# Optimization experiments

Hardware: AMD Instinct MI355X
Metric: run time of the kernel (lower is better)

## Reference

```python
import jax, jax.numpy as jnp
import numpy as np

E = 768
H = 12
D = E // H          # head_dim = 64
R = 4               # reduced_head_dim
SCALING = D ** -0.5  # scaling_factor = 1
B, T = 4, 1024


def setup_inputs() -> dict:
    key = jax.random.key(0)
    ks = jax.random.split(key, 12)
    query = jax.random.normal(ks[0], (B, T, E), dtype=jnp.float32)
    k_dynamic_T = jax.random.normal(ks[1], (B * H * T, R, T), dtype=jnp.float32)
    kpm = jax.random.bernoulli(ks[2], 0.2, (B, T))
    kpm = kpm.at[:, 0].set(False)  # keep at least one key unmasked per row
    attn_bias = jax.random.normal(ks[3], (B * H, T, T), dtype=jnp.float32)
    s_in = (2.0 / (E + 3 * E)) ** 0.5
    s_red = (2.0 / (D + R)) ** 0.5
    s_out = (2.0 / (E + E)) ** 0.5
    return {
        "query": query,
        "k_dynamic_T": k_dynamic_T,
        "key_padding_mask": kpm,
        "attn_bias": attn_bias,
        "in_w": jax.random.normal(ks[4], (3 * E, E), dtype=jnp.float32) * s_in,
        "in_b": jax.random.normal(ks[5], (3 * E,), dtype=jnp.float32) * 0.02,
        "red_w": jax.random.normal(ks[6], (R, D), dtype=jnp.float32) * s_red,
        "red_b": jax.random.normal(ks[7], (R,), dtype=jnp.float32) * 0.02,
        "out_w": jax.random.normal(ks[8], (E, E), dtype=jnp.float32) * s_out,
        "out_b": jax.random.normal(ks[9], (E,), dtype=jnp.float32) * 0.02,
    }


def reference(query, k_dynamic_T, key_padding_mask, attn_bias,
              in_w, in_b, red_w, red_b, out_w, out_b):
    bsz, tgt_len, _ = query.shape
    # QKV projection (torch Linear: x @ W.T + b)
    qkv = jnp.einsum("bte,fe->btf", query, in_w) + in_b
    q, k, v = jnp.split(qkv, 3, axis=-1)
    # [B, H, T, D]
    q = q.reshape(bsz, tgt_len, H, D).transpose(0, 2, 1, 3)
    k = k.reshape(bsz, tgt_len, H, D).transpose(0, 2, 1, 3)
    v = v.reshape(bsz, tgt_len, H, D).transpose(0, 2, 1, 3)
    # low-rank dynamic bias: q_reduced from UNSCALED q
    q_red = jnp.einsum("bhtd,rd->bhtr", q, red_w) + red_b          # [B,H,T,R]
    k_dyn = k_dynamic_T.reshape(bsz, H, tgt_len, R, tgt_len)       # [B,H,T,R,S]
    attn_dyn = jnp.einsum("bhtr,bhtrs->bhts", q_red, k_dyn)        # [B,H,T,S]
    # scaled dot-product scores + dynamic bias
    scores = jnp.einsum("bhtd,bhsd->bhts", q * SCALING, k) + attn_dyn
    # key padding mask -> -inf
    scores = jnp.where(key_padding_mask[:, None, None, :], -jnp.inf, scores)
    # attn_bias added inside softmax_dropout (bias arg); dropout inactive (eval)
    scores = scores + attn_bias.reshape(bsz, H, tgt_len, tgt_len)
    attn = jax.nn.softmax(scores, axis=-1)
    o = jnp.einsum("bhts,bhsd->bhtd", attn, v)                     # [B,H,T,D]
    o = o.transpose(0, 2, 1, 3).reshape(bsz, tgt_len, E)
    return jnp.einsum("bte,fe->btf", o, out_w) + out_b
```

## Files before the change

kernel.cpp:

```cpp
#include <hip/hip_runtime.h>
#include <math.h>

typedef __attribute__((ext_vector_type(8))) short s16x8;
typedef __attribute__((ext_vector_type(4))) float f32x4;

#define MFMA(a,b,c) __builtin_amdgcn_mfma_f32_16x16x32_bf16((a),(b),(c),0,0,0)

__device__ __forceinline__ unsigned short f2bf(float f){
    unsigned u = __builtin_bit_cast(unsigned, f);
    u += 0x7FFFu + ((u >> 16) & 1u);
    return (unsigned short)(u >> 16);
}
__device__ __forceinline__ float bf2f(unsigned short u){
    return __builtin_bit_cast(float, ((unsigned)u) << 16);
}
__device__ __forceinline__ float4 fma4(float s, float4 a, float4 c){
    c.x = fmaf(s, a.x, c.x); c.y = fmaf(s, a.y, c.y);
    c.z = fmaf(s, a.z, c.z); c.w = fmaf(s, a.w, c.w);
    return c;
}
__device__ __forceinline__ unsigned pk_bf16(float lo, float hi){
    return (unsigned)f2bf(lo) | ((unsigned)f2bf(hi) << 16);
}
__device__ __forceinline__ void gld_lds16(const void* g, void* l){
    __builtin_amdgcn_global_load_lds(
        (const __attribute__((address_space(1))) void*)g,
        (__attribute__((address_space(3))) void*)l, 16, 0, 0);
}

__global__ __launch_bounds__(256) void cvt3(
    const float* __restrict__ s0, unsigned short* __restrict__ d0, int n0,
    const float* __restrict__ s1, unsigned short* __restrict__ d1, int n1,
    const float* __restrict__ s2, unsigned short* __restrict__ d2, int n2)
{
    const int i = blockIdx.x*256 + threadIdx.x;
    const float* s; unsigned short* d; int j;
    if (i < n0){ s = s0; d = d0; j = i; }
    else if (i < n0 + n1){ s = s1; d = d1; j = i - n0; }
    else if (i < n0 + n1 + n2){ s = s2; d = d2; j = i - n0 - n1; }
    else return;
    float4 a = *(const float4*)(s + (size_t)j*8);
    float4 b = *(const float4*)(s + (size_t)j*8 + 4);
    alignas(16) unsigned short t[8] = {
        f2bf(a.x), f2bf(a.y), f2bf(a.z), f2bf(a.w),
        f2bf(b.x), f2bf(b.y), f2bf(b.z), f2bf(b.w) };
    *(s16x8*)(d + (size_t)j*8) = *(const s16x8*)t;
}

__global__ __launch_bounds__(256) void gemm_qkv_bf16(
    const unsigned short* __restrict__ X,
    const unsigned short* __restrict__ W,
    const float* __restrict__ bvec,
    unsigned short* __restrict__ qs,
    unsigned short* __restrict__ kb,
    unsigned short* __restrict__ vtb)
{
    __shared__ __align__(16) unsigned short Al[128*64];
    __shared__ __align__(16) unsigned short Bl[128*64];
    const int tid = threadIdx.x;
    const int m0 = blockIdx.y*128, n0 = blockIdx.x*128;
    const int w = tid>>6, lane = tid&63, g = lane>>4, cc = lane&15;
    const int arow_base = (w>>1)*64, brow_base = (w&1)*64;
    const int srowb = w*32 + (lane>>3);
    const int gl = lane&7;

    f32x4 acc[4][4];
#pragma unroll
    for (int i=0;i<4;i++)
#pragma unroll
        for (int j=0;j<4;j++) acc[i][j] = (f32x4){0.f,0.f,0.f,0.f};

    for (int kt = 0; kt < 768; kt += 64) {
        __syncthreads();
#pragma unroll
        for (int i=0;i<4;i++){
            const int ra = srowb + i*8;
            gld_lds16(X + (size_t)(m0+ra)*768 + kt + ((gl ^ (ra&7))<<3),
                      &Al[(w*32 + i*8)*64]);
            gld_lds16(W + (size_t)(n0+ra)*768 + kt + ((gl ^ (ra&7))<<3),
                      &Bl[(w*32 + i*8)*64]);
        }
        __syncthreads();
#pragma unroll
        for (int ks=0;ks<2;ks++){
            s16x8 af[4], bfr[4];
#pragma unroll
            for (int i=0;i<4;i++){
                const int ra = arow_base + i*16 + cc;
                const int rb = brow_base + i*16 + cc;
                af[i]  = *(const s16x8*)&Al[ra*64 + (((ks*4+g) ^ (ra&7))<<3)];
                bfr[i] = *(const s16x8*)&Bl[rb*64 + (((ks*4+g) ^ (rb&7))<<3)];
            }
#pragma unroll
            for (int i=0;i<4;i++)
#pragma unroll
                for (int j=0;j<4;j++)
                    acc[i][j] = MFMA(af[i], bfr[j], acc[i][j]);
        }
    }

    const int region = blockIdx.x / 6;
#pragma unroll
    for (int j=0;j<4;j++){
        const int n = n0 + brow_base + j*16 + cc;
        const float bb = bvec[n];
        const int nn = n - region*768;
        const int h = nn >> 6, d = nn & 63;
        if (region == 0){
#pragma unroll
            for (int i=0;i<4;i++){
                const int m = m0 + arow_base + i*16 + g*4;
                const int bq = m >> 10, t = m & 1023;
                unsigned short* dst = qs + ((size_t)(bq*12+h)*1024 + t)*64 + d;
#pragma unroll
                for (int r=0;r<4;r++)
                    dst[(size_t)r*64] = f2bf((acc[i][j][r] + bb)*0.125f);
            }
        } else if (region == 1){
#pragma unroll
            for (int i=0;i<4;i++){
                const int m = m0 + arow_base + i*16 + g*4;
                const int bq = m >> 10, t = m & 1023;
                unsigned short* dst = kb + ((size_t)(bq*12+h)*1024 + t)*64 + d;
#pragma unroll
                for (int r=0;r<4;r++)
                    dst[(size_t)r*64] = f2bf(acc[i][j][r] + bb);
            }
        } else {
#pragma unroll
            for (int i=0;i<4;i++){
                const int m = m0 + arow_base + i*16 + g*4;
                const int bq = m >> 10, t = m & 1023;
                ushort4 pk;
                pk.x = f2bf(acc[i][j][0] + bb);
                pk.y = f2bf(acc[i][j][1] + bb);
                pk.z = f2bf(acc[i][j][2] + bb);
                pk.w = f2bf(acc[i][j][3] + bb);
                *(ushort4*)&vtb[((size_t)(bq*12+h)*64 + d)*1024 + t] = pk;
            }
        }
    }
}

__global__ __launch_bounds__(256) void gemm_obf_bf16(
    const unsigned short* __restrict__ X,
    const unsigned short* __restrict__ W,
    const float* __restrict__ bvec, float* __restrict__ out)
{
    __shared__ __align__(16) unsigned short Al[128*64];
    __shared__ __align__(16) unsigned short Bl[128*64];
    const int tid = threadIdx.x;
    const int m0 = blockIdx.y*128, n0 = blockIdx.x*128;
    const int w = tid>>6, lane = tid&63, g = lane>>4, cc = lane&15;
    const int arow_base = (w>>1)*64, brow_base = (w&1)*64;
    const int srowb = w*32 + (lane>>3);
    const int gl = lane&7;

    f32x4 acc[4][4];
#pragma unroll
    for (int i=0;i<4;i++)
#pragma unroll
        for (int j=0;j<4;j++) acc[i][j] = (f32x4){0.f,0.f,0.f,0.f};

    for (int kt = 0; kt < 768; kt += 64) {
        __syncthreads();
#pragma unroll
        for (int i=0;i<4;i++){
            const int ra = srowb + i*8;
            gld_lds16(X + (size_t)(m0+ra)*768 + kt + ((gl ^ (ra&7))<<3),
                      &Al[(w*32 + i*8)*64]);
            gld_lds16(W + (size_t)(n0+ra)*768 + kt + ((gl ^ (ra&7))<<3),
                      &Bl[(w*32 + i*8)*64]);
        }
        __syncthreads();
#pragma unroll
        for (int ks=0;ks<2;ks++){
            s16x8 af[4], bfr[4];
#pragma unroll
            for (int i=0;i<4;i++){
                const int ra = arow_base + i*16 + cc;
                const int rb = brow_base + i*16 + cc;
                af[i]  = *(const s16x8*)&Al[ra*64 + (((ks*4+g) ^ (ra&7))<<3)];
                bfr[i] = *(const s16x8*)&Bl[rb*64 + (((ks*4+g) ^ (rb&7))<<3)];
            }
#pragma unroll
            for (int i=0;i<4;i++)
#pragma unroll
                for (int j=0;j<4;j++)
                    acc[i][j] = MFMA(af[i], bfr[j], acc[i][j]);
        }
    }
#pragma unroll
    for (int j=0;j<4;j++){
        const int n = n0 + brow_base + j*16 + cc;
        const float bb = bvec[n];
#pragma unroll
        for (int i=0;i<4;i++){
            const int mb = m0 + arow_base + i*16 + g*4;
#pragma unroll
            for (int r=0;r<4;r++)
                out[(size_t)(mb+r)*768 + n] = acc[i][j][r] + bb;
        }
    }
}

__global__ __launch_bounds__(64, 1) void attn_mfma(
    const unsigned short* __restrict__ qs,
    const unsigned short* __restrict__ kbf,
    const unsigned short* __restrict__ vtf,
    const float* __restrict__ kdyn,
    const int*   __restrict__ kpm,
    const float* __restrict__ bias,
    const float* __restrict__ red_w,
    const float* __restrict__ red_b,
    unsigned short* __restrict__ o)
{
    __shared__ __align__(16) float kdL[2][2048];
    __shared__ __align__(16) float bL[2][512];

    const int lane = threadIdx.x & 63;
    const int bh = blockIdx.x, qt = blockIdx.y;
    const int b = bh / 12, h = bh % 12;
    const int t0 = qt*16;
    const int g = lane>>4, cc = lane&15;
    const int tq = t0 + cc;

    const unsigned short* qrow = qs + ((size_t)bh*1024 + tq)*64;
    s16x8 qf[2];
    qf[0] = *(const s16x8*)(qrow + g*8);
    qf[1] = *(const s16x8*)(qrow + 32 + g*8);

    float qred[4];
    {
        float pr[4] = {0.f,0.f,0.f,0.f};
#pragma unroll
        for (int ks=0; ks<2; ks++){
#pragma unroll
            for (int r=0;r<4;r++){
                float4 w0 = *(const float4*)(red_w + r*64 + 32*ks + 8*g);
                float4 w1 = *(const float4*)(red_w + r*64 + 32*ks + 8*g + 4);
                pr[r] += bf2f((unsigned short)qf[ks][0])*w0.x + bf2f((unsigned short)qf[ks][1])*w0.y
                       + bf2f((unsigned short)qf[ks][2])*w0.z + bf2f((unsigned short)qf[ks][3])*w0.w
                       + bf2f((unsigned short)qf[ks][4])*w1.x + bf2f((unsigned short)qf[ks][5])*w1.y
                       + bf2f((unsigned short)qf[ks][6])*w1.z + bf2f((unsigned short)qf[ks][7])*w1.w;
            }
        }
#pragma unroll
        for (int r=0;r<4;r++){
            pr[r] += __shfl_xor(pr[r], 16);
            pr[r] += __shfl_xor(pr[r], 32);
            qred[r] = pr[r]*8.f + red_b[r];
        }
    }

    f32x4 accO[4];
#pragma unroll
    for (int i=0;i<4;i++) accO[i] = (f32x4){0.f,0.f,0.f,0.f};
    float m_ = -1e30f, l_ = 0.f;

    const unsigned short* kcb = kbf + (size_t)bh*1024*64;
    const unsigned short* vcb = vtf + ((size_t)bh*64 + cc)*1024;
    const int* mp = kpm + b*1024 + 4*g;
    const size_t kd_row = (size_t)(bh*1024 + t0);

    const int r8_ = lane>>3, g8_ = lane&7;

    #define STAGE(buf_, c_) do {                                                  \
        const int s0_ = (c_)*32;                                                  \
        _Pragma("unroll")                                                         \
        for (int i_=0;i_<8;i_++){                         \
            const int rr_ = 8*i_ + r8_;                                           \
            const int t_ = rr_>>2, r_ = rr_&3;                                    \
            gld_lds16(kdyn + (kd_row + t_)*4096 + (size_t)r_*1024 + s0_           \
                          + ((g8_ ^ (t_&7))<<2),                                  \
                      &kdL[buf_][i_*256]);                                        \
        }                                                                         \
        _Pragma("unroll")                                                         \
        for (int i_=0;i_<2;i_++){                          \
            const int t_ = 8*i_ + r8_;                                            \
            gld_lds16(bias + (kd_row + t_)*1024 + s0_ + ((g8_ ^ (t_&7))<<2),      \
                      &bL[buf_][i_*256]);                                         \
        }                                                                         \
    } while(0)

    STAGE(0, 0);

    const float NINF = -__builtin_inff();
    const int srcA = ((g&1)<<5) + cc;
    const int srcB = srcA + 16;
    const bool hi_half = (g>>1) != 0;

#pragma unroll 1
    for (int c = 0; c < 32; ++c) {
        const int buf = c & 1;
        const int s0 = c*32;

        s16x8 kfr[2][2];
#pragma unroll
        for (int sq=0;sq<2;sq++){
            const unsigned short* kp = kcb + (size_t)(s0 + 16*sq + cc)*64 + g*8;
            kfr[sq][0] = *(const s16x8*)(kp);
            kfr[sq][1] = *(const s16x8*)(kp + 32);
        }
        s16x8 vfr[4];
#pragma unroll
        for (int dq=0;dq<4;dq++)
            vfr[dq] = *(const s16x8*)(vcb + (size_t)dq*16*1024 + s0 + 8*g);
        int4 mm0 = *(const int4*)(mp + s0);
        int4 mm1 = *(const int4*)(mp + s0 + 16);
        __builtin_amdgcn_sched_barrier(0);

        if (c < 31){
            STAGE(buf^1, c+1);
            asm volatile("s_waitcnt vmcnt(10)" ::: "memory");
        } else {
            asm volatile("s_waitcnt vmcnt(0)" ::: "memory");
        }
        __builtin_amdgcn_sched_barrier(0);

        float4 dyn[2];
#pragma unroll
        for (int sq=0;sq<2;sq++){
            const int slot = ((4*sq + g) ^ (cc&7)) << 2;
            float4 dv = *(const float4*)&bL[buf][cc*32 + slot];
            dv = fma4(qred[0], *(const float4*)&kdL[buf][(cc*4+0)*32 + slot], dv);
            dv = fma4(qred[1], *(const float4*)&kdL[buf][(cc*4+1)*32 + slot], dv);
            dv = fma4(qred[2], *(const float4*)&kdL[buf][(cc*4+2)*32 + slot], dv);
            dv = fma4(qred[3], *(const float4*)&kdL[buf][(cc*4+3)*32 + slot], dv);
            const int4 m4 = sq ? mm1 : mm0;
            dv.x = m4.x ? NINF : dv.x;
            dv.y = m4.y ? NINF : dv.y;
            dv.z = m4.z ? NINF : dv.z;
            dv.w = m4.w ? NINF : dv.w;
            dyn[sq] = dv;
        }

        f32x4 sc[2];
        __builtin_amdgcn_s_setprio(1);
#pragma unroll
        for (int sq=0;sq<2;sq++){
            f32x4 z = (f32x4){0.f,0.f,0.f,0.f};
            z = MFMA(kfr[sq][0], qf[0], z);
            z = MFMA(kfr[sq][1], qf[1], z);
            sc[sq] = z;
        }
        __builtin_amdgcn_s_setprio(0);

        float v[8];
#pragma unroll
        for (int sq=0;sq<2;sq++){
            v[sq*4+0] = sc[sq][0] + dyn[sq].x;
            v[sq*4+1] = sc[sq][1] + dyn[sq].y;
            v[sq*4+2] = sc[sq][2] + dyn[sq].z;
            v[sq*4+3] = sc[sq][3] + dyn[sq].w;
        }
        float mx = v[0];
#pragma unroll
        for (int i=1;i<8;i++) mx = fmaxf(mx, v[i]);
        mx = fmaxf(mx, __shfl_xor(mx, 16));
        mx = fmaxf(mx, __shfl_xor(mx, 32));
        const float mn = fmaxf(m_, mx);
        float ps = 0.f;
#pragma unroll
        for (int i=0;i<8;i++){ v[i] = __expf(v[i]-mn); ps += v[i]; }
        ps += __shfl_xor(ps, 16);
        ps += __shfl_xor(ps, 32);
        const float scl = __expf(m_-mn);
        m_ = mn; l_ = l_*scl + ps;

        unsigned U[4] = { pk_bf16(v[0],v[1]), pk_bf16(v[2],v[3]),
                          pk_bf16(v[4],v[5]), pk_bf16(v[6],v[7]) };
        unsigned a0 = (unsigned)__shfl((int)U[0], srcA);
        unsigned a1 = (unsigned)__shfl((int)U[1], srcA);
        unsigned a2 = (unsigned)__shfl((int)U[2], srcA);
        unsigned a3 = (unsigned)__shfl((int)U[3], srcA);
        unsigned b0 = (unsigned)__shfl((int)U[0], srcB);
        unsigned b1 = (unsigned)__shfl((int)U[1], srcB);
        unsigned b2 = (unsigned)__shfl((int)U[2], srcB);
        unsigned b3 = (unsigned)__shfl((int)U[3], srcB);
        alignas(16) unsigned wv4[4] = { hi_half ? a2 : a0, hi_half ? a3 : a1,
                                        hi_half ? b2 : b0, hi_half ? b3 : b1 };
        s16x8 pa = *(const s16x8*)wv4;

        float sr[4];
#pragma unroll
        for (int r=0;r<4;r++) sr[r] = __shfl(scl, 20*g + r);
#pragma unroll
        for (int dq=0;dq<4;dq++){
            f32x4 a = accO[dq];
            a[0]*=sr[0]; a[1]*=sr[1]; a[2]*=sr[2]; a[3]*=sr[3];
            accO[dq] = a;
        }

        __builtin_amdgcn_s_setprio(1);
#pragma unroll
        for (int dq=0;dq<4;dq++)
            accO[dq] = MFMA(pa, vfr[dq], accO[dq]);
        __builtin_amdgcn_s_setprio(0);
    }
    #undef STAGE

    float linv[4];
#pragma unroll
    for (int r=0;r<4;r++) linv[r] = 1.0f / __shfl(l_, 20*g + r);
#pragma unroll
    for (int dq=0;dq<4;dq++){
#pragma unroll
        for (int r=0;r<4;r++){
            const int t = t0 + 4*g + r;
            o[(size_t)(b*1024 + t)*768 + h*64 + 16*dq + cc] = f2bf(accO[dq][r] * linv[r]);
        }
    }
}

extern "C" void kernel_launch(void* const* d_in, const int* in_sizes, int n_in,
                              void* d_out, int out_size, void* d_ws, size_t ws_size,
                              hipStream_t stream) {
    const float* query = (const float*)d_in[0];
    const float* kdyn  = (const float*)d_in[1];
    const int*   kpm   = (const int*)d_in[2];
    const float* bias  = (const float*)d_in[3];
    const float* in_w  = (const float*)d_in[4];
    const float* in_b  = (const float*)d_in[5];
    const float* red_w = (const float*)d_in[6];
    const float* red_b = (const float*)d_in[7];
    const float* out_w = (const float*)d_in[8];
    const float* out_b = (const float*)d_in[9];
    float* out = (float*)d_out;

    const size_t SEG = (size_t)48*1024*64;
    unsigned short* qs  = (unsigned short*)d_ws;
    unsigned short* kb  = qs + SEG;
    unsigned short* vt  = kb + SEG;
    unsigned short* ob  = vt + SEG;
    unsigned short* qb  = ob + SEG;
    unsigned short* wqb = qb + SEG;
    unsigned short* wob = wqb + (size_t)2304*768;

    const int n0 = (4096*768)/8;
    const int n1 = (2304*768)/8;
    const int n2 = (768*768)/8;
    cvt3<<<dim3((n0+n1+n2+255)/256), 256, 0, stream>>>(
        query, qb, n0, in_w, wqb, n1, out_w, wob, n2);

    gemm_qkv_bf16<<<dim3(18,32), 256, 0, stream>>>(qb, wqb, in_b, qs, kb, vt);
    attn_mfma<<<dim3(48,64), 64, 0, stream>>>(qs, kb, vt, kdyn, kpm, bias, red_w, red_b, ob);
    gemm_obf_bf16<<<dim3(6,32), 256, 0, stream>>>(ob, wob, out_b, out);
}
```

Measured before the change: 284.5 us.

## Double-buffer LDS tiles in QKV and output projection GEMMs

Both projection GEMMs now keep two LDS buffers per operand. The next k-tile is loaded directly into LDS while MFMAs run on the current one, synchronized with explicit vmcnt waits and barriers. This is meant to hide global-load latency behind compute, which the single-buffered loop exposed every iteration. LDS use per block doubles to 64 KB, which may lower occupancy. The hand-placed waitcnt counts also assume exactly 8 outstanding loads per stage.

```diff
diff --git a/kernel.cpp b/kernel.cpp
--- a/kernel.cpp
+++ b/kernel.cpp
@@ -55,8 +55,8 @@
     unsigned short* __restrict__ kb,
     unsigned short* __restrict__ vtb)
 {
-    __shared__ __align__(16) unsigned short Al[128*64];
-    __shared__ __align__(16) unsigned short Bl[128*64];
+    __shared__ __align__(16) unsigned short Al[2][128*64];
+    __shared__ __align__(16) unsigned short Bl[2][128*64];
     const int tid = threadIdx.x;
     const int m0 = blockIdx.y*128, n0 = blockIdx.x*128;
     const int w = tid>>6, lane = tid&63, g = lane>>4, cc = lane&15;
@@ -70,17 +70,28 @@
 #pragma unroll
         for (int j=0;j<4;j++) acc[i][j] = (f32x4){0.f,0.f,0.f,0.f};
 
-    for (int kt = 0; kt < 768; kt += 64) {
-        __syncthreads();
-#pragma unroll
-        for (int i=0;i<4;i++){
-            const int ra = srowb + i*8;
-            gld_lds16(X + (size_t)(m0+ra)*768 + kt + ((gl ^ (ra&7))<<3),
-                      &Al[(w*32 + i*8)*64]);
-            gld_lds16(W + (size_t)(n0+ra)*768 + kt + ((gl ^ (ra&7))<<3),
-                      &Bl[(w*32 + i*8)*64]);
-        }
-        __syncthreads();
+    #define GSTAGE(buf_, kt_) do {                                          \
+        _Pragma("unroll")                                                   \
+        for (int i_=0;i_<4;i_++){                                           \
+            const int ra_ = srowb + i_*8;                                   \
+            gld_lds16(X + (size_t)(m0+ra_)*768 + (kt_) + ((gl ^ (ra_&7))<<3), \
+                      &Al[buf_][(w*32 + i_*8)*64]);                         \
+            gld_lds16(W + (size_t)(n0+ra_)*768 + (kt_) + ((gl ^ (ra_&7))<<3), \
+                      &Bl[buf_][(w*32 + i_*8)*64]);                         \
+        }                                                                   \
+    } while(0)
+
+    GSTAGE(0, 0);
+    for (int step = 0; step < 12; ++step){
+        const int buf = step & 1;
+        if (step < 11){
+            GSTAGE(buf^1, (step+1)*64);
+            asm volatile("s_waitcnt vmcnt(8)" ::: "memory");
+        } else {
+            asm volatile("s_waitcnt vmcnt(0)" ::: "memory");
+        }
+        __builtin_amdgcn_s_barrier();
+        __builtin_amdgcn_sched_barrier(0);
 #pragma unroll
         for (int ks=0;ks<2;ks++){
             s16x8 af[4], bfr[4];
@@ -88,8 +99,8 @@
             for (int i=0;i<4;i++){
                 const int ra = arow_base + i*16 + cc;
                 const int rb = brow_base + i*16 + cc;
-                af[i]  = *(const s16x8*)&Al[ra*64 + (((ks*4+g) ^ (ra&7))<<3)];
-                bfr[i] = *(const s16x8*)&Bl[rb*64 + (((ks*4+g) ^ (rb&7))<<3)];
+                af[i]  = *(const s16x8*)&Al[buf][ra*64 + (((ks*4+g) ^ (ra&7))<<3)];
+                bfr[i] = *(const s16x8*)&Bl[buf][rb*64 + (((ks*4+g) ^ (rb&7))<<3)];
             }
 #pragma unroll
             for (int i=0;i<4;i++)
@@ -97,7 +108,10 @@
                 for (int j=0;j<4;j++)
                     acc[i][j] = MFMA(af[i], bfr[j], acc[i][j]);
         }
-    }
+        asm volatile("s_waitcnt lgkmcnt(0)" ::: "memory");
+        __builtin_amdgcn_s_barrier();
+    }
+    #undef GSTAGE
 
     const int region = blockIdx.x / 6;
 #pragma unroll
@@ -147,8 +161,8 @@
     const unsigned short* __restrict__ W,
     const float* __restrict__ bvec, float* __restrict__ out)
 {
-    __shared__ __align__(16) unsigned short Al[128*64];
-    __shared__ __align__(16) unsigned short Bl[128*64];
+    __shared__ __align__(16) unsigned short Al[2][128*64];
+    __shared__ __align__(16) unsigned short Bl[2][128*64];
     const int tid = threadIdx.x;
     const int m0 = blockIdx.y*128, n0 = blockIdx.x*128;
     const int w = tid>>6, lane = tid&63, g = lane>>4, cc = lane&15;
@@ -162,17 +176,28 @@
 #pragma unroll
         for (int j=0;j<4;j++) acc[i][j] = (f32x4){0.f,0.f,0.f,0.f};
 
-    for (int kt = 0; kt < 768; kt += 64) {
-        __syncthreads();
-#pragma unroll
-        for (int i=0;i<4;i++){
-            const int ra = srowb + i*8;
-            gld_lds16(X + (size_t)(m0+ra)*768 + kt + ((gl ^ (ra&7))<<3),
-                      &Al[(w*32 + i*8)*64]);
-            gld_lds16(W + (size_t)(n0+ra)*768 + kt + ((gl ^ (ra&7))<<3),
-                      &Bl[(w*32 + i*8)*64]);
-        }
-        __syncthreads();
+    #define GSTAGE(buf_, kt_) do {                                          \
+        _Pragma("unroll")                                                   \
+        for (int i_=0;i_<4;i_++){                                           \
+            const int ra_ = srowb + i_*8;                                   \
+            gld_lds16(X + (size_t)(m0+ra_)*768 + (kt_) + ((gl ^ (ra_&7))<<3), \
+                      &Al[buf_][(w*32 + i_*8)*64]);                         \
+            gld_lds16(W + (size_t)(n0+ra_)*768 + (kt_) + ((gl ^ (ra_&7))<<3), \
+                      &Bl[buf_][(w*32 + i_*8)*64]);                         \
+        }                                                                   \
+    } while(0)
+
+    GSTAGE(0, 0);
+    for (int step = 0; step < 12; ++step){
+        const int buf = step & 1;
+        if (step < 11){
+            GSTAGE(buf^1, (step+1)*64);
+            asm volatile("s_waitcnt vmcnt(8)" ::: "memory");
+        } else {
+            asm volatile("s_waitcnt vmcnt(0)" ::: "memory");
+        }
+        __builtin_amdgcn_s_barrier();
+        __builtin_amdgcn_sched_barrier(0);
 #pragma unroll
         for (int ks=0;ks<2;ks++){
             s16x8 af[4], bfr[4];
@@ -180,8 +205,8 @@
             for (int i=0;i<4;i++){
                 const int ra = arow_base + i*16 + cc;
                 const int rb = brow_base + i*16 + cc;
-                af[i]  = *(const s16x8*)&Al[ra*64 + (((ks*4+g) ^ (ra&7))<<3)];
-                bfr[i] = *(const s16x8*)&Bl[rb*64 + (((ks*4+g) ^ (rb&7))<<3)];
+                af[i]  = *(const s16x8*)&Al[buf][ra*64 + (((ks*4+g) ^ (ra&7))<<3)];
+                bfr[i] = *(const s16x8*)&Bl[buf][rb*64 + (((ks*4+g) ^ (rb&7))<<3)];
             }
 #pragma unroll
             for (int i=0;i<4;i++)
@@ -189,7 +214,11 @@
                 for (int j=0;j<4;j++)
                     acc[i][j] = MFMA(af[i], bfr[j], acc[i][j]);
         }
-    }
+        asm volatile("s_waitcnt lgkmcnt(0)" ::: "memory");
+        __builtin_amdgcn_s_barrier();
+    }
+    #undef GSTAGE
+
 #pragma unroll
     for (int j=0;j<4;j++){
         const int n = n0 + brow_base + j*16 + cc;
```

New measurement: 303.4 us. +6.7%, slower.

## Double-buffer K/V/mask register loads one chunk ahead in attention loop

Applied to the files above, without the earlier changes.

The K and V fragment loads and the key-padding mask loads move out of the current iteration and are prefetched into double-buffered registers for the next chunk, alongside the existing LDS staging of the dynamic-bias and attention-bias tiles. The waitcnt threshold is raised to cover the extra in-flight loads, so global latency for K/V overlaps with compute. The loop is unrolled by 2 so the register buffers can be indexed statically, and launch bounds now ask for 2 blocks per CU. The extra register buffers raise VGPR pressure and could cause spills or limit occupancy.

```diff
diff --git a/kernel.cpp b/kernel.cpp
--- a/kernel.cpp
+++ b/kernel.cpp
@@ -204,7 +204,7 @@
     }
 }
 
-__global__ __launch_bounds__(64, 1) void attn_mfma(
+__global__ __launch_bounds__(64, 2) void attn_mfma(
     const unsigned short* __restrict__ qs,
     const unsigned short* __restrict__ kbf,
     const unsigned short* __restrict__ vtf,
@@ -283,6 +283,26 @@
         }                                                                         \
     } while(0)
 
+    #define REGLOAD(p_, c_) do {                                                  \
+        const int s0n_ = (c_)*32;                                                 \
+        _Pragma("unroll")                                                         \
+        for (int sq_=0;sq_<2;sq_++){                                              \
+            const unsigned short* kp_ = kcb + (size_t)(s0n_ + 16*sq_ + cc)*64 + g*8; \
+            kfr[p_][sq_][0] = *(const s16x8*)(kp_);                               \
+            kfr[p_][sq_][1] = *(const s16x8*)(kp_ + 32);                          \
+        }                                                                         \
+        _Pragma("unroll")                                                         \
+        for (int dq_=0;dq_<4;dq_++)                                               \
+            vfr[p_][dq_] = *(const s16x8*)(vcb + (size_t)dq_*16*1024 + s0n_ + 8*g); \
+        mm0r[p_] = *(const int4*)(mp + s0n_);                                     \
+        mm1r[p_] = *(const int4*)(mp + s0n_ + 16);                                \
+    } while(0)
+
+    s16x8 kfr[2][2][2];
+    s16x8 vfr[2][4];
+    int4 mm0r[2], mm1r[2];
+
+    REGLOAD(0, 0);
     STAGE(0, 0);
 
     const float NINF = -__builtin_inff();
@@ -290,29 +310,14 @@
     const int srcB = srcA + 16;
     const bool hi_half = (g>>1) != 0;
 
-#pragma unroll 1
+#pragma unroll 2
     for (int c = 0; c < 32; ++c) {
-        const int buf = c & 1;
-        const int s0 = c*32;
-
-        s16x8 kfr[2][2];
-#pragma unroll
-        for (int sq=0;sq<2;sq++){
-            const unsigned short* kp = kcb + (size_t)(s0 + 16*sq + cc)*64 + g*8;
-            kfr[sq][0] = *(const s16x8*)(kp);
-            kfr[sq][1] = *(const s16x8*)(kp + 32);
-        }
-        s16x8 vfr[4];
-#pragma unroll
-        for (int dq=0;dq<4;dq++)
-            vfr[dq] = *(const s16x8*)(vcb + (size_t)dq*16*1024 + s0 + 8*g);
-        int4 mm0 = *(const int4*)(mp + s0);
-        int4 mm1 = *(const int4*)(mp + s0 + 16);
-        __builtin_amdgcn_sched_barrier(0);
+        const int pb = c & 1;
 
         if (c < 31){
-            STAGE(buf^1, c+1);
-            asm volatile("s_waitcnt vmcnt(10)" ::: "memory");
+            REGLOAD(pb^1, c+1);
+            STAGE(pb^1, c+1);
+            asm volatile("s_waitcnt vmcnt(20)" ::: "memory");
         } else {
             asm volatile("s_waitcnt vmcnt(0)" ::: "memory");
         }
@@ -322,12 +327,12 @@
 #pragma unroll
         for (int sq=0;sq<2;sq++){
             const int slot = ((4*sq + g) ^ (cc&7)) << 2;
-            float4 dv = *(const float4*)&bL[buf][cc*32 + slot];
-            dv = fma4(qred[0], *(const float4*)&kdL[buf][(cc*4+0)*32 + slot], dv);
-            dv = fma4(qred[1], *(const float4*)&kdL[buf][(cc*4+1)*32 + slot], dv);
-            dv = fma4(qred[2], *(const float4*)&kdL[buf][(cc*4+2)*32 + slot], dv);
-            dv = fma4(qred[3], *(const float4*)&kdL[buf][(cc*4+3)*32 + slot], dv);
-            const int4 m4 = sq ? mm1 : mm0;
+            float4 dv = *(const float4*)&bL[pb][cc*32 + slot];
+            dv = fma4(qred[0], *(const float4*)&kdL[pb][(cc*4+0)*32 + slot], dv);
+            dv = fma4(qred[1], *(const float4*)&kdL[pb][(cc*4+1)*32 + slot], dv);
+            dv = fma4(qred[2], *(const float4*)&kdL[pb][(cc*4+2)*32 + slot], dv);
+            dv = fma4(qred[3], *(const float4*)&kdL[pb][(cc*4+3)*32 + slot], dv);
+            const int4 m4 = sq ? mm1r[pb] : mm0r[pb];
             dv.x = m4.x ? NINF : dv.x;
             dv.y = m4.y ? NINF : dv.y;
             dv.z = m4.z ? NINF : dv.z;
@@ -340,8 +345,8 @@
 #pragma unroll
         for (int sq=0;sq<2;sq++){
             f32x4 z = (f32x4){0.f,0.f,0.f,0.f};
-            z = MFMA(kfr[sq][0], qf[0], z);
-            z = MFMA(kfr[sq][1], qf[1], z);
+            z = MFMA(kfr[pb][sq][0], qf[0], z);
+            z = MFMA(kfr[pb][sq][1], qf[1], z);
             sc[sq] = z;
         }
         __builtin_amdgcn_s_setprio(0);
@@ -395,10 +400,11 @@
         __builtin_amdgcn_s_setprio(1);
 #pragma unroll
         for (int dq=0;dq<4;dq++)
-            accO[dq] = MFMA(pa, vfr[dq], accO[dq]);
+            accO[dq] = MFMA(pa, vfr[pb][dq], accO[dq]);
         __builtin_amdgcn_s_setprio(0);
     }
     #undef STAGE
+    #undef REGLOAD
 
     float linv[4];
 #pragma unroll
```

Measured after the change: 283.5 us. Within noise of the previous version (-0.3%).
